# Kernel optimization log

Hardware: AMD Instinct MI355X
Metric: run time of the kernel (lower is better)

The kernel has to match this reference:

```python
import jax, jax.numpy as jnp
import numpy as np

N_NODES = 100000
N_EDGES = 600000
NODE_IN = 387
HID = 128
EDGE_DIM = 7


def _p(key, shape, scale=0.02):
    return jax.random.normal(key, shape, dtype=jnp.float32) * scale


def setup_inputs() -> dict:
    key = jax.random.key(0)
    ks = jax.random.split(key, 24)
    x = jax.random.normal(ks[0], (N_NODES, NODE_IN), dtype=jnp.float32)
    edge_index = jax.random.randint(ks[1], (2, N_EDGES), 0, N_NODES, dtype=jnp.int64)
    edge_attr = jax.random.normal(ks[2], (N_EDGES, EDGE_DIM), dtype=jnp.float32)
    return {
        "x": x,
        "edge_index": edge_index,
        "edge_attr": edge_attr,
        # conv1: edge lin (7 -> 387), mlp (387 -> 128 -> 128)
        "e1_w": _p(ks[3], (EDGE_DIM, NODE_IN)), "e1_b": jnp.zeros((NODE_IN,), jnp.float32),
        "m1_w1": _p(ks[4], (NODE_IN, HID)), "m1_b1": jnp.zeros((HID,), jnp.float32),
        "m1_w2": _p(ks[5], (HID, HID)), "m1_b2": jnp.zeros((HID,), jnp.float32),
        # conv2: edge lin (7 -> 128), mlp (128 -> 128 -> 128)
        "e2_w": _p(ks[6], (EDGE_DIM, HID)), "e2_b": jnp.zeros((HID,), jnp.float32),
        "m2_w1": _p(ks[7], (HID, HID)), "m2_b1": jnp.zeros((HID,), jnp.float32),
        "m2_w2": _p(ks[8], (HID, HID)), "m2_b2": jnp.zeros((HID,), jnp.float32),
        # edge_mlp: (2*128+7 -> 128 -> 2); dropout is identity at eval
        "em_w1": _p(ks[9], (2 * HID + EDGE_DIM, HID)), "em_b1": jnp.zeros((HID,), jnp.float32),
        "em_w2": _p(ks[10], (HID, 2)), "em_b2": jnp.zeros((2,), jnp.float32),
    }


def gine_conv(x, src, dst, edge_attr, ew, eb, w1, b1, w2, b2, eps=0.0):
    # message: relu(x_j + Lin(edge_attr)); aggregate sum at destination
    msg = jax.nn.relu(x[src] + edge_attr @ ew + eb)  # [E, D]
    aggr = jax.ops.segment_sum(msg, dst, num_segments=x.shape[0])  # [N, D]
    h = (1.0 + eps) * x + aggr
    return jax.nn.relu(h @ w1 + b1) @ w2 + b2


def reference(x, edge_index, edge_attr,
              e1_w, e1_b, m1_w1, m1_b1, m1_w2, m1_b2,
              e2_w, e2_b, m2_w1, m2_b1, m2_w2, m2_b2,
              em_w1, em_b1, em_w2, em_b2):
    src, dst = edge_index[0], edge_index[1]
    h = gine_conv(x, src, dst, edge_attr, e1_w, e1_b, m1_w1, m1_b1, m1_w2, m1_b2)
    h = jax.nn.relu(h)
    h = gine_conv(h, src, dst, edge_attr, e2_w, e2_b, m2_w1, m2_b1, m2_w2, m2_b2)
    h = jax.nn.relu(h)
    edge_input = jnp.concatenate([h[src], h[dst], edge_attr], axis=1)  # [E, 263]
    return jax.nn.relu(edge_input @ em_w1 + em_b1) @ em_w2 + em_b2  # [E, 2]
```

## Files before the change

kernel.cpp:

```cpp
#include <hip/hip_runtime.h>


using f32x4 = __attribute__((ext_vector_type(4))) float;
using s16x8 = __attribute__((ext_vector_type(8))) short;

#define N_NODES 100000
#define N_EDGES 600000
#define NODE_IN 387
#define KPAD    416
#define HID     128
#define NB_SCAN 391

__device__ __forceinline__ unsigned short f2bf(float f) {
    unsigned u = __float_as_uint(f);
    u += 0x7FFFu + ((u >> 16) & 1u);
    return (unsigned short)(u >> 16);
}
__device__ __forceinline__ float bf2f(short h) {
    return __uint_as_float(((unsigned)(unsigned short)h) << 16);
}

__global__ __launch_bounds__(256) void k_decode(const unsigned* __restrict__ w,
                                                int* __restrict__ s32,
                                                int* __restrict__ d32) {
    __shared__ unsigned long long bs[4];
    __shared__ int is64_s;
    const int t = threadIdx.x;
    unsigned any = 0;
    for (int i = 1 + 2 * t; i < 2048; i += 512) any |= w[i];
    unsigned long long b = __ballot(any != 0);
    if ((t & 63) == 0) bs[t >> 6] = b;
    __syncthreads();
    if (t == 0) is64_s = ((bs[0] | bs[1] | bs[2] | bs[3]) == 0ULL) ? 1 : 0;
    __syncthreads();
    const int is64 = is64_s;
    const int e = blockIdx.x * 256 + t;
    if (e < N_EDGES) {
        if (is64) {
            s32[e] = (int)w[2 * e];
            d32[e] = (int)w[2 * N_EDGES + 2 * e];
        } else {
            s32[e] = (int)w[e];
            d32[e] = (int)w[N_EDGES + e];
        }
    }
}

__global__ __launch_bounds__(256) void k_prep(const float* __restrict__ w1,
                                              const float* __restrict__ w2,
                                              const float* __restrict__ v1,
                                              const float* __restrict__ v2,
                                              const float* __restrict__ ew1,
                                              unsigned short* __restrict__ W1t,
                                              unsigned short* __restrict__ W2t,
                                              unsigned short* __restrict__ V1t,
                                              unsigned short* __restrict__ V2t,
                                              unsigned short* __restrict__ EW1t) {
    int i = blockIdx.x * 256 + threadIdx.x;
    if (i < 128 * KPAD) {
        int c = i / KPAD, k = i - c * KPAD;
        W1t[i] = (k < NODE_IN) ? f2bf(w1[k * HID + c]) : (unsigned short)0;
        return;
    }
    i -= 128 * KPAD;
    if (i < 16384) { int c = i >> 7, k = i & 127; W2t[i] = f2bf(w2[k * HID + c]); return; }
    i -= 16384;
    if (i < 16384) { int c = i >> 7, k = i & 127; V1t[i] = f2bf(v1[k * HID + c]); return; }
    i -= 16384;
    if (i < 16384) { int c = i >> 7, k = i & 127; V2t[i] = f2bf(v2[k * HID + c]); return; }
    i -= 16384;
    if (i < 32768) { int c = i >> 8, k = i & 255; EW1t[i] = f2bf(ew1[k * HID + c]); return; }
}

__global__ __launch_bounds__(256) void k_castx(const float* __restrict__ x,
                                               unsigned short* __restrict__ xbf) {
    const int g = blockIdx.x * 256 + threadIdx.x;
    if (g >= N_NODES * 52) return;
    const int row = g / 52, c0 = (g - row * 52) * 8;
    s16x8 v;
#pragma unroll
    for (int j = 0; j < 8; ++j) {
        const int c = c0 + j;
        v[j] = (c < NODE_IN) ? (short)f2bf(x[row * NODE_IN + c]) : (short)0;
    }
    *(s16x8*)&xbf[row * KPAD + c0] = v;
}

__global__ __launch_bounds__(256) void k_hist(const int* __restrict__ d32,
                                              int* __restrict__ cnt) {
    const int e = blockIdx.x * 256 + threadIdx.x;
    if (e < N_EDGES) atomicAdd(&cnt[d32[e]], 1);
}

__global__ __launch_bounds__(256) void k_scanA(const int* __restrict__ cnt,
                                               int* __restrict__ bsum) {
    __shared__ int wt[4];
    const int t = threadIdx.x;
    const int i = blockIdx.x * 256 + t;
    int v = (i < N_NODES) ? cnt[i] : 0;
#pragma unroll
    for (int off = 32; off; off >>= 1) v += __shfl_down(v, off);
    if ((t & 63) == 0) wt[t >> 6] = v;
    __syncthreads();
    if (t == 0) bsum[blockIdx.x] = wt[0] + wt[1] + wt[2] + wt[3];
}

__global__ __launch_bounds__(256) void k_scanC(int* __restrict__ cnt,
                                               const int* __restrict__ bsum) {
    __shared__ int wt[4];
    __shared__ int wt2[4];
    __shared__ int sh_bofs;
    const int t = threadIdx.x, b = blockIdx.x;
    int accp = 0;
    for (int i = t; i < NB_SCAN; i += 256) if (i < b) accp += bsum[i];
#pragma unroll
    for (int off = 32; off; off >>= 1) accp += __shfl_down(accp, off);
    if ((t & 63) == 0) wt[t >> 6] = accp;
    __syncthreads();
    if (t == 0) sh_bofs = wt[0] + wt[1] + wt[2] + wt[3];
    const int i = b * 256 + t;
    const int v = (i < N_NODES) ? cnt[i] : 0;
    int inc = v;
    const int lane = t & 63;
#pragma unroll
    for (int off = 1; off < 64; off <<= 1) {
        int u = __shfl_up(inc, off);
        if (lane >= off) inc += u;
    }
    if (lane == 63) wt2[t >> 6] = inc;
    __syncthreads();
    int wbase = 0;
    for (int wI = 0; wI < (t >> 6); ++wI) wbase += wt2[wI];
    if (i < N_NODES) cnt[i] = sh_bofs + wbase + inc - v;
}

__global__ __launch_bounds__(256) void k_scatter(const int* __restrict__ s32,
                                                 const int* __restrict__ d32,
                                                 const float* __restrict__ ea,
                                                 int* __restrict__ cur,
                                                 int* __restrict__ ss2,
                                                 int* __restrict__ ds2,
                                                 float* __restrict__ eas) {
    const int e = blockIdx.x * 256 + threadIdx.x;
    if (e < N_EDGES) {
        const int d = d32[e];
        const int pos = atomicAdd(&cur[d], 1);
        ss2[pos] = s32[e];
        ds2[pos] = d;
#pragma unroll
        for (int q = 0; q < 7; ++q) eas[pos * 8 + q] = ea[e * 7 + q];
        eas[pos * 8 + 7] = 0.f;
    }
}

#define STAGE_B(dst, srcbase, stride_) do {                                   \
    const int col_ = t >> 1, h_ = t & 1;                                      \
    *(s16x8*)&(dst)[col_ * 40 + h_ * 16] =                                    \
        *(const s16x8*)&(srcbase)[col_ * (stride_) + h_ * 16];                \
    *(s16x8*)&(dst)[col_ * 40 + h_ * 16 + 8] =                                \
        *(const s16x8*)&(srcbase)[col_ * (stride_) + h_ * 16 + 8];            \
} while (0)

__global__ __launch_bounds__(256) void k_edge1(const unsigned short* __restrict__ xbf,
                                               const int* __restrict__ ss2,
                                               const int* __restrict__ ds2,
                                               const float* __restrict__ eas,
                                               const float* __restrict__ e1w,
                                               const float* __restrict__ e1b,
                                               const unsigned short* __restrict__ W1t,
                                               float* __restrict__ yagg) {
    __shared__ __align__(16) char pool[31232];
    unsigned short* Asm = (unsigned short*)(pool);
    unsigned short* Bsm = (unsigned short*)(pool + 5120);
    float* e1w_s = (float*)(pool + 15360);
    float* e1b_s = (float*)(pool + 27008);
    float* ea_s  = (float*)(pool + 28672);
    int* ss_s    = (int*)(pool + 30720);
    int* dst_s   = (int*)(pool + 30976);
    float* Csm   = (float*)(pool);

    const int t = threadIdx.x;
    const int e0 = blockIdx.x * 64;

    if (t < 64) ss_s[t] = ss2[e0 + t];
    else if (t < 128) dst_s[t - 64] = ds2[e0 + (t - 64)];
    for (int i = t; i < 7 * KPAD; i += 256) {
        int q = i / KPAD, k = i - q * KPAD;
        e1w_s[i] = (k < NODE_IN) ? e1w[q * NODE_IN + k] : 0.f;
    }
    for (int i = t; i < KPAD; i += 256) e1b_s[i] = (i < NODE_IN) ? e1b[i] : 0.f;
    for (int i = t; i < 512; i += 256) ea_s[i] = eas[e0 * 8 + i];
    __syncthreads();

    const int lane = t & 63, wid = t >> 6;
    const int wr = wid >> 1, wc = wid & 1;
    const int r = t >> 2, kc = (t & 3) * 8;
    const int srow = ss_s[r];
    float eav[7];
#pragma unroll
    for (int q = 0; q < 7; ++q) eav[q] = ea_s[r * 8 + q];

    f32x4 acc[2][4];
    const f32x4 zero = {0.f, 0.f, 0.f, 0.f};
#pragma unroll
    for (int mi = 0; mi < 2; ++mi)
#pragma unroll
        for (int ni = 0; ni < 4; ++ni) acc[mi][ni] = zero;

    s16x8 xa_n = *(const s16x8*)&xbf[srow * KPAD + kc];
    for (int ks = 0; ks < 13; ++ks) {
        const s16x8 xa = xa_n;
        if (ks < 12) xa_n = *(const s16x8*)&xbf[srow * KPAD + (ks + 1) * 32 + kc];
        {
            const int kb = ks * 32 + kc;
            s16x8 v;
#pragma unroll
            for (int j = 0; j < 8; ++j) {
                const int k = kb + j;
                float le = e1b_s[k];
#pragma unroll
                for (int q = 0; q < 7; ++q) le = fmaf(eav[q], e1w_s[q * KPAD + k], le);
                v[j] = (short)f2bf(fmaxf(bf2f(xa[j]) + le, 0.f));
            }
            *(s16x8*)&Asm[r * 40 + kc] = v;
        }
        STAGE_B(Bsm, &W1t[ks * 32], KPAD);
        __syncthreads();
        const int koff = (lane >> 4) * 8;
        const int rA = lane & 15;
        s16x8 a0 = *(const s16x8*)&Asm[(wr * 32 + rA) * 40 + koff];
        s16x8 a1 = *(const s16x8*)&Asm[(wr * 32 + 16 + rA) * 40 + koff];
#pragma unroll
        for (int ni = 0; ni < 4; ++ni) {
            s16x8 b = *(const s16x8*)&Bsm[(wc * 64 + ni * 16 + rA) * 40 + koff];
            acc[0][ni] = __builtin_amdgcn_mfma_f32_16x16x32_bf16(a0, b, acc[0][ni], 0, 0, 0);
            acc[1][ni] = __builtin_amdgcn_mfma_f32_16x16x32_bf16(a1, b, acc[1][ni], 0, 0, 0);
        }
        __syncthreads();
    }
    const int g = lane >> 4;
    const int cb = wc * 64 + (lane & 15);
#pragma unroll
    for (int p = 0; p < 2; ++p) {
        if (wr == p) {
#pragma unroll
            for (int mi = 0; mi < 2; ++mi)
#pragma unroll
                for (int reg = 0; reg < 4; ++reg) {
                    const int row = mi * 16 + g * 4 + reg;
#pragma unroll
                    for (int ni = 0; ni < 4; ++ni)
                        Csm[row * 129 + cb + ni * 16] = acc[mi][ni][reg];
                }
        }
        __syncthreads();
        if (t < 128) {
            const int base = p * 32;
            float s = 0.f;
            int prev = dst_s[base];
            for (int rr = 0; rr < 32; ++rr) {
                const int d = dst_s[base + rr];
                const float v = Csm[rr * 129 + t];
                if (d != prev) { atomicAdd(&yagg[prev * HID + t], s); s = 0.f; prev = d; }
                s += v;
            }
            atomicAdd(&yagg[prev * HID + t], s);
        }
        __syncthreads();
    }
}

__global__ __launch_bounds__(256) void k_node1(const unsigned short* __restrict__ xbf,
                                               const float* __restrict__ yagg,
                                               const unsigned short* __restrict__ W1t,
                                               const unsigned short* __restrict__ W2t,
                                               const float* __restrict__ b1,
                                               const float* __restrict__ b2,
                                               unsigned short* __restrict__ r1b) {
    __shared__ __align__(16) unsigned short Asm[64 * 40];
    __shared__ __align__(16) unsigned short Bsm[128 * 40];
    __shared__ __align__(16) unsigned short Hsm[64 * 136];
    const int t = threadIdx.x;
    const int i0 = blockIdx.x * 64;
    const int lane = t & 63, wid = t >> 6, wr = wid >> 1, wc = wid & 1;
    const int r = t >> 2, kc = (t & 3) * 8;
    const int rg = i0 + r;
    const bool rvalid = rg < N_NODES;

    f32x4 acc[2][4];
    const f32x4 zero = {0.f, 0.f, 0.f, 0.f};
#pragma unroll
    for (int mi = 0; mi < 2; ++mi)
#pragma unroll
        for (int ni = 0; ni < 4; ++ni) acc[mi][ni] = zero;

    for (int ks = 0; ks < 13; ++ks) {
        {
            s16x8 v;
            if (rvalid) v = *(const s16x8*)&xbf[rg * KPAD + ks * 32 + kc];
            else {
#pragma unroll
                for (int j = 0; j < 8; ++j) v[j] = 0;
            }
            *(s16x8*)&Asm[r * 40 + kc] = v;
        }
        STAGE_B(Bsm, &W1t[ks * 32], KPAD);
        __syncthreads();
        const int koff = (lane >> 4) * 8;
        const int rA = lane & 15;
        s16x8 a0 = *(const s16x8*)&Asm[(wr * 32 + rA) * 40 + koff];
        s16x8 a1 = *(const s16x8*)&Asm[(wr * 32 + 16 + rA) * 40 + koff];
#pragma unroll
        for (int ni = 0; ni < 4; ++ni) {
            s16x8 b = *(const s16x8*)&Bsm[(wc * 64 + ni * 16 + rA) * 40 + koff];
            acc[0][ni] = __builtin_amdgcn_mfma_f32_16x16x32_bf16(a0, b, acc[0][ni], 0, 0, 0);
            acc[1][ni] = __builtin_amdgcn_mfma_f32_16x16x32_bf16(a1, b, acc[1][ni], 0, 0, 0);
        }
        __syncthreads();
    }
    const int jb = wc * 64 + (lane & 15);
#pragma unroll
    for (int mi = 0; mi < 2; ++mi) {
#pragma unroll
        for (int reg = 0; reg < 4; ++reg) {
            const int rloc = wr * 32 + mi * 16 + (lane >> 4) * 4 + reg;
            const int rowg = i0 + rloc;
#pragma unroll
            for (int ni = 0; ni < 4; ++ni) {
                const int j = jb + ni * 16;
                float v = acc[mi][ni][reg];
                if (rowg < N_NODES) {
                    v += yagg[rowg * HID + j] + b1[j];
                    v = fmaxf(v, 0.f);
                } else v = 0.f;
                Hsm[rloc * 136 + j] = f2bf(v);
            }
        }
    }
    __syncthreads();
    f32x4 acc2[2][4];
#pragma unroll
    for (int mi = 0; mi < 2; ++mi)
#pragma unroll
        for (int ni = 0; ni < 4; ++ni) acc2[mi][ni] = zero;

    for (int ks = 0; ks < 4; ++ks) {
        STAGE_B(Bsm, &W2t[ks * 32], HID);
        __syncthreads();
        const int koff = (lane >> 4) * 8;
        const int rA = lane & 15;
        s16x8 a0 = *(const s16x8*)&Hsm[(wr * 32 + rA) * 136 + ks * 32 + koff];
        s16x8 a1 = *(const s16x8*)&Hsm[(wr * 32 + 16 + rA) * 136 + ks * 32 + koff];
#pragma unroll
        for (int ni = 0; ni < 4; ++ni) {
            s16x8 b = *(const s16x8*)&Bsm[(wc * 64 + ni * 16 + rA) * 40 + koff];
            acc2[0][ni] = __builtin_amdgcn_mfma_f32_16x16x32_bf16(a0, b, acc2[0][ni], 0, 0, 0);
            acc2[1][ni] = __builtin_amdgcn_mfma_f32_16x16x32_bf16(a1, b, acc2[1][ni], 0, 0, 0);
        }
        __syncthreads();
    }
#pragma unroll
    for (int mi = 0; mi < 2; ++mi) {
#pragma unroll
        for (int reg = 0; reg < 4; ++reg) {
            const int rloc = wr * 32 + mi * 16 + (lane >> 4) * 4 + reg;
            const int rowg = i0 + rloc;
            if (rowg < N_NODES) {
#pragma unroll
                for (int ni = 0; ni < 4; ++ni) {
                    const int j = jb + ni * 16;
                    float v = acc2[mi][ni][reg] + b2[j];
                    r1b[rowg * HID + j] = f2bf(fmaxf(v, 0.f));
                }
            }
        }
    }
}

__global__ __launch_bounds__(256) void k_edge2(const unsigned short* __restrict__ r1b,
                                               const int* __restrict__ ss2,
                                               const int* __restrict__ ds2,
                                               const float* __restrict__ eas,
                                               const float* __restrict__ e2w,
                                               const float* __restrict__ e2b,
                                               float* __restrict__ agg2) {
    __shared__ float w_s[7 * HID];
    __shared__ float b_s[HID];
    __shared__ float Csm[64 * 129];
    __shared__ float ea_s[64 * 8];
    __shared__ int ss_s[64];
    __shared__ int ds_s[64];
    const int t = threadIdx.x;
    const int e0 = blockIdx.x * 64;
    for (int i = t; i < 7 * HID; i += 256) w_s[i] = e2w[i];
    if (t < HID) b_s[t] = e2b[t];
    if (t < 64) ss_s[t] = ss2[e0 + t];
    else if (t < 128) ds_s[t - 64] = ds2[e0 + (t - 64)];
    for (int i = t; i < 512; i += 256) ea_s[i] = eas[e0 * 8 + i];
    __syncthreads();

    const int r = t >> 2, c0 = (t & 3) * 32;
    const int s = ss_s[r];
    float eav[7];
#pragma unroll
    for (int q = 0; q < 7; ++q) eav[q] = ea_s[r * 8 + q];
    const s16x8* rp = (const s16x8*)&r1b[s * HID + c0];
#pragma unroll
    for (int u = 0; u < 4; ++u) {
        s16x8 hv = rp[u];
#pragma unroll
        for (int j = 0; j < 8; ++j) {
            const int c = c0 + u * 8 + j;
            float v = bf2f(hv[j]) + b_s[c];
#pragma unroll
            for (int q = 0; q < 7; ++q) v = fmaf(eav[q], w_s[q * HID + c], v);
            Csm[r * 129 + c] = fmaxf(v, 0.f);
        }
    }
    __syncthreads();
    if (t < 128) {
        float ssum = 0.f;
        int prev = ds_s[0];
        for (int rr = 0; rr < 64; ++rr) {
            const int d = ds_s[rr];
            const float v = Csm[rr * 129 + t];
            if (d != prev) { atomicAdd(&agg2[prev * HID + t], ssum); ssum = 0.f; prev = d; }
            ssum += v;
        }
        atomicAdd(&agg2[prev * HID + t], ssum);
    }
}

__global__ __launch_bounds__(256) void k_node2(const unsigned short* __restrict__ r1b,
                                               const float* __restrict__ agg2,
                                               const unsigned short* __restrict__ V1t,
                                               const unsigned short* __restrict__ V2t,
                                               const float* __restrict__ b1,
                                               const float* __restrict__ b2,
                                               unsigned short* __restrict__ r2) {
    __shared__ __align__(16) unsigned short Asm[64 * 40];
    __shared__ __align__(16) unsigned short Bsm[128 * 40];
    __shared__ __align__(16) unsigned short Hsm[64 * 136];
    const int t = threadIdx.x;
    const int i0 = blockIdx.x * 64;
    const int lane = t & 63, wid = t >> 6, wr = wid >> 1, wc = wid & 1;
    const int r = t >> 2, kc = (t & 3) * 8;
    const int rg = i0 + r;
    const bool rvalid = rg < N_NODES;

    f32x4 acc[2][4];
    const f32x4 zero = {0.f, 0.f, 0.f, 0.f};
#pragma unroll
    for (int mi = 0; mi < 2; ++mi)
#pragma unroll
        for (int ni = 0; ni < 4; ++ni) acc[mi][ni] = zero;

    for (int ks = 0; ks < 4; ++ks) {
        {
            const int kb = ks * 32 + kc;
            s16x8 v;
            if (rvalid) {
                const s16x8 ra = *(const s16x8*)&r1b[rg * HID + kb];
                const f32x4* pb = (const f32x4*)&agg2[rg * HID + kb];
                f32x4 w0 = pb[0], w1 = pb[1];
#pragma unroll
                for (int j = 0; j < 4; ++j) v[j] = (short)f2bf(bf2f(ra[j]) + w0[j]);
#pragma unroll
                for (int j = 0; j < 4; ++j) v[4 + j] = (short)f2bf(bf2f(ra[4 + j]) + w1[j]);
            } else {
#pragma unroll
                for (int j = 0; j < 8; ++j) v[j] = 0;
            }
            *(s16x8*)&Asm[r * 40 + kc] = v;
        }
        STAGE_B(Bsm, &V1t[ks * 32], HID);
        __syncthreads();
        const int koff = (lane >> 4) * 8;
        const int rA = lane & 15;
        s16x8 a0 = *(const s16x8*)&Asm[(wr * 32 + rA) * 40 + koff];
        s16x8 a1 = *(const s16x8*)&Asm[(wr * 32 + 16 + rA) * 40 + koff];
#pragma unroll
        for (int ni = 0; ni < 4; ++ni) {
            s16x8 b = *(const s16x8*)&Bsm[(wc * 64 + ni * 16 + rA) * 40 + koff];
            acc[0][ni] = __builtin_amdgcn_mfma_f32_16x16x32_bf16(a0, b, acc[0][ni], 0, 0, 0);
            acc[1][ni] = __builtin_amdgcn_mfma_f32_16x16x32_bf16(a1, b, acc[1][ni], 0, 0, 0);
        }
        __syncthreads();
    }
    const int jb = wc * 64 + (lane & 15);
#pragma unroll
    for (int mi = 0; mi < 2; ++mi) {
#pragma unroll
        for (int reg = 0; reg < 4; ++reg) {
            const int rloc = wr * 32 + mi * 16 + (lane >> 4) * 4 + reg;
            const int rowg = i0 + rloc;
#pragma unroll
            for (int ni = 0; ni < 4; ++ni) {
                const int j = jb + ni * 16;
                float v = acc[mi][ni][reg];
                if (rowg < N_NODES) {
                    v += b1[j];
                    v = fmaxf(v, 0.f);
                } else v = 0.f;
                Hsm[rloc * 136 + j] = f2bf(v);
            }
        }
    }
    __syncthreads();
    f32x4 acc2[2][4];
#pragma unroll
    for (int mi = 0; mi < 2; ++mi)
#pragma unroll
        for (int ni = 0; ni < 4; ++ni) acc2[mi][ni] = zero;

    for (int ks = 0; ks < 4; ++ks) {
        STAGE_B(Bsm, &V2t[ks * 32], HID);
        __syncthreads();
        const int koff = (lane >> 4) * 8;
        const int rA = lane & 15;
        s16x8 a0 = *(const s16x8*)&Hsm[(wr * 32 + rA) * 136 + ks * 32 + koff];
        s16x8 a1 = *(const s16x8*)&Hsm[(wr * 32 + 16 + rA) * 136 + ks * 32 + koff];
#pragma unroll
        for (int ni = 0; ni < 4; ++ni) {
            s16x8 b = *(const s16x8*)&Bsm[(wc * 64 + ni * 16 + rA) * 40 + koff];
            acc2[0][ni] = __builtin_amdgcn_mfma_f32_16x16x32_bf16(a0, b, acc2[0][ni], 0, 0, 0);
            acc2[1][ni] = __builtin_amdgcn_mfma_f32_16x16x32_bf16(a1, b, acc2[1][ni], 0, 0, 0);
        }
        __syncthreads();
    }
#pragma unroll
    for (int mi = 0; mi < 2; ++mi) {
#pragma unroll
        for (int reg = 0; reg < 4; ++reg) {
            const int rloc = wr * 32 + mi * 16 + (lane >> 4) * 4 + reg;
            const int rowg = i0 + rloc;
            if (rowg < N_NODES) {
#pragma unroll
                for (int ni = 0; ni < 4; ++ni) {
                    const int j = jb + ni * 16;
                    float v = acc2[mi][ni][reg] + b2[j];
                    r2[rowg * HID + j] = f2bf(fmaxf(v, 0.f));
                }
            }
        }
    }
}

__global__ __launch_bounds__(256) void k_head(const unsigned short* __restrict__ r2,
                                              const int* __restrict__ srcp,
                                              const int* __restrict__ dstp,
                                              const float* __restrict__ ea,
                                              const unsigned short* __restrict__ EW1t,
                                              const float* __restrict__ emw1,
                                              const float* __restrict__ emb1,
                                              const float* __restrict__ emw2,
                                              const float* __restrict__ emb2,
                                              float* __restrict__ out) {
    __shared__ __align__(16) unsigned short Asm[64 * 40];
    __shared__ __align__(16) unsigned short Bsm[128 * 40];
    __shared__ float Hsm[64 * 129];
    __shared__ float ew_ea[7 * HID];
    __shared__ float eb1_s[HID];
    __shared__ float w2_s[256];
    __shared__ float b2_s[2];
    __shared__ float ea_s[64 * 8];
    __shared__ int src_s[64];
    __shared__ int dst_s[64];
    __shared__ float red[512];
    const int t = threadIdx.x;
    const int e0 = blockIdx.x * 64;

    for (int i = t; i < 7 * HID; i += 256) ew_ea[i] = emw1[256 * HID + i];
    if (t < HID) eb1_s[t] = emb1[t];
    if (t < 256) w2_s[t] = emw2[t];
    if (t < 2) b2_s[t] = emb2[t];
    for (int i = t; i < 64 * 7; i += 256) {
        int r = i / 7, q = i - r * 7;
        ea_s[r * 8 + q] = ea[(e0 + r) * 7 + q];
    }
    if (t < 64) src_s[t] = srcp[e0 + t];
    else if (t < 128) dst_s[t - 64] = dstp[e0 + (t - 64)];
    __syncthreads();

    const int lane = t & 63, wid = t >> 6, wr = wid >> 1, wc = wid & 1;
    const int r = t >> 2, kc = (t & 3) * 8;

    f32x4 acc[2][4];
    const f32x4 zero = {0.f, 0.f, 0.f, 0.f};
#pragma unroll
    for (int mi = 0; mi < 2; ++mi)
#pragma unroll
        for (int ni = 0; ni < 4; ++ni) acc[mi][ni] = zero;

    for (int ks = 0; ks < 8; ++ks) {
        {
            const int k = ks * 32 + kc;
            const unsigned short* p = (k < HID) ? &r2[src_s[r] * HID + k]
                                                : &r2[dst_s[r] * HID + (k - HID)];
            *(s16x8*)&Asm[r * 40 + kc] = *(const s16x8*)p;
        }
        STAGE_B(Bsm, &EW1t[ks * 32], 256);
        __syncthreads();
        const int koff = (lane >> 4) * 8;
        const int rA = lane & 15;
        s16x8 a0 = *(const s16x8*)&Asm[(wr * 32 + rA) * 40 + koff];
        s16x8 a1 = *(const s16x8*)&Asm[(wr * 32 + 16 + rA) * 40 + koff];
#pragma unroll
        for (int ni = 0; ni < 4; ++ni) {
            s16x8 b = *(const s16x8*)&Bsm[(wc * 64 + ni * 16 + rA) * 40 + koff];
            acc[0][ni] = __builtin_amdgcn_mfma_f32_16x16x32_bf16(a0, b, acc[0][ni], 0, 0, 0);
            acc[1][ni] = __builtin_amdgcn_mfma_f32_16x16x32_bf16(a1, b, acc[1][ni], 0, 0, 0);
        }
        __syncthreads();
    }
    const int jb = wc * 64 + (lane & 15);
#pragma unroll
    for (int mi = 0; mi < 2; ++mi) {
#pragma unroll
        for (int reg = 0; reg < 4; ++reg) {
            const int rloc = wr * 32 + mi * 16 + (lane >> 4) * 4 + reg;
#pragma unroll
            for (int ni = 0; ni < 4; ++ni) {
                const int j = jb + ni * 16;
                float v = acc[mi][ni][reg] + eb1_s[j];
#pragma unroll
                for (int q = 0; q < 7; ++q)
                    v = fmaf(ea_s[rloc * 8 + q], ew_ea[q * HID + j], v);
                Hsm[rloc * 129 + j] = fmaxf(v, 0.f);
            }
        }
    }
    __syncthreads();
    {
        const int e = t & 63, p = t >> 6;
        const float* hb = &Hsm[e * 129 + p * 32];
        float s0 = 0.f, s1 = 0.f;
#pragma unroll
        for (int j = 0; j < 32; ++j) {
            const float h = hb[j];
            s0 = fmaf(h, w2_s[(p * 32 + j) * 2], s0);
            s1 = fmaf(h, w2_s[(p * 32 + j) * 2 + 1], s1);
        }
        red[(e * 4 + p) * 2] = s0;
        red[(e * 4 + p) * 2 + 1] = s1;
    }
    __syncthreads();
    if (t < 64) {
        float o0 = b2_s[0], o1 = b2_s[1];
#pragma unroll
        for (int p = 0; p < 4; ++p) {
            o0 += red[(t * 4 + p) * 2];
            o1 += red[(t * 4 + p) * 2 + 1];
        }
        out[(e0 + t) * 2] = o0;
        out[(e0 + t) * 2 + 1] = o1;
    }
}

extern "C" void kernel_launch(void* const* d_in, const int* in_sizes, int n_in,
                              void* d_out, int out_size, void* d_ws, size_t ws_size,
                              hipStream_t stream) {
    (void)in_sizes; (void)n_in; (void)out_size; (void)ws_size;
    const float* x    = (const float*)d_in[0];
    const unsigned* eidx = (const unsigned*)d_in[1];
    const float* ea   = (const float*)d_in[2];
    const float* e1w  = (const float*)d_in[3];
    const float* e1b  = (const float*)d_in[4];
    const float* m1w1 = (const float*)d_in[5];
    const float* m1b1 = (const float*)d_in[6];
    const float* m1w2 = (const float*)d_in[7];
    const float* m1b2 = (const float*)d_in[8];
    const float* e2w  = (const float*)d_in[9];
    const float* e2b  = (const float*)d_in[10];
    const float* m2w1 = (const float*)d_in[11];
    const float* m2b1 = (const float*)d_in[12];
    const float* m2w2 = (const float*)d_in[13];
    const float* m2b2 = (const float*)d_in[14];
    const float* emw1 = (const float*)d_in[15];
    const float* emb1 = (const float*)d_in[16];
    const float* emw2 = (const float*)d_in[17];
    const float* emb2 = (const float*)d_in[18];
    float* out = (float*)d_out;

    char* ws = (char*)d_ws;
    float* yagg = (float*)(ws + 0);
    unsigned short* r1b = (unsigned short*)(ws + 51200000);
    unsigned short* r2  = (unsigned short*)(ws + 76800000);
    float* eas          = (float*)(ws + 76800000);
    unsigned short* xbf = (unsigned short*)(ws + 102400000);
    unsigned short* W1t  = (unsigned short*)(ws + 185600000);
    unsigned short* W2t  = (unsigned short*)(ws + 185706496);
    unsigned short* V1t  = (unsigned short*)(ws + 185739264);
    unsigned short* V2t  = (unsigned short*)(ws + 185772032);
    unsigned short* EW1t = (unsigned short*)(ws + 185804800);
    int* s32  = (int*)(ws + 185870336);
    int* d32  = (int*)(ws + 188270336);
    int* ss2  = (int*)(ws + 190670336);
    int* ds2  = (int*)(ws + 193070336);
    int* cnt  = (int*)(ws + 195470336);
    int* bsum = (int*)(ws + 195870336);

    hipMemsetAsync(yagg, 0, (size_t)N_NODES * HID * 4, stream);
    hipMemsetAsync(cnt, 0, (size_t)N_NODES * 4, stream);
    k_decode<<<2344, 256, 0, stream>>>(eidx, s32, d32);
    k_prep<<<528, 256, 0, stream>>>(m1w1, m1w2, m2w1, m2w2, emw1, W1t, W2t, V1t, V2t, EW1t);
    k_castx<<<(N_NODES * 52 + 255) / 256, 256, 0, stream>>>(x, xbf);
    k_hist<<<2344, 256, 0, stream>>>(d32, cnt);
    k_scanA<<<NB_SCAN, 256, 0, stream>>>(cnt, bsum);
    k_scanC<<<NB_SCAN, 256, 0, stream>>>(cnt, bsum);
    k_scatter<<<2344, 256, 0, stream>>>(s32, d32, ea, cnt, ss2, ds2, eas);
    k_edge1<<<N_EDGES / 64, 256, 0, stream>>>(xbf, ss2, ds2, eas, e1w, e1b, W1t, yagg);
    k_node1<<<(N_NODES + 63) / 64, 256, 0, stream>>>(xbf, yagg, W1t, W2t, m1b1, m1b2, r1b);
    hipMemsetAsync(yagg, 0, (size_t)N_NODES * HID * 4, stream);
    k_edge2<<<N_EDGES / 64, 256, 0, stream>>>(r1b, ss2, ds2, eas, e2w, e2b, yagg);
    k_node2<<<(N_NODES + 63) / 64, 256, 0, stream>>>(r1b, yagg, V1t, V2t, m2b1, m2b2, r2);
    k_head<<<N_EDGES / 64, 256, 0, stream>>>(r2, s32, d32, ea, EW1t, emw1, emb1, emw2, emb2, out);
}
```

Measured before the change: 1.076 ms.

## Compute edge-attr linear terms with MFMA instead of scalar FMA loops

Packs the 7-wide edge-attribute weights plus bias into padded bf16 matrices in the prep kernel. In k_edge1 and k_head, the per-element scalar FMA loops over edge attributes are replaced with small MFMA products, using an augmented [ea, 1] row so the bias is folded in. This removes the per-block staging of fp32 edge weights and a lot of VALU work. It also splits the segmented atomic reduction in k_edge1 across all 256 threads instead of 128. The cost is extra syncs per k-step and bf16 rounding of the edge-attr weights and bias, which were fp32 before.

Result: faster. 924.6 us (-14.1%).

```diff
diff --git a/kernel.cpp b/kernel.cpp
--- a/kernel.cpp
+++ b/kernel.cpp
@@ -51,11 +51,16 @@
                                               const float* __restrict__ v1,
                                               const float* __restrict__ v2,
                                               const float* __restrict__ ew1,
+                                              const float* __restrict__ e1w,
+                                              const float* __restrict__ e1b,
+                                              const float* __restrict__ emb1,
                                               unsigned short* __restrict__ W1t,
                                               unsigned short* __restrict__ W2t,
                                               unsigned short* __restrict__ V1t,
                                               unsigned short* __restrict__ V2t,
-                                              unsigned short* __restrict__ EW1t) {
+                                              unsigned short* __restrict__ EW1t,
+                                              unsigned short* __restrict__ E1T,
+                                              unsigned short* __restrict__ EWeaT) {
     int i = blockIdx.x * 256 + threadIdx.x;
     if (i < 128 * KPAD) {
         int c = i / KPAD, k = i - c * KPAD;
@@ -70,6 +75,26 @@
     if (i < 16384) { int c = i >> 7, k = i & 127; V2t[i] = f2bf(v2[k * HID + c]); return; }
     i -= 16384;
     if (i < 32768) { int c = i >> 8, k = i & 255; EW1t[i] = f2bf(ew1[k * HID + c]); return; }
+    i -= 32768;
+    if (i < 416 * 32) {
+        int f = i >> 5, q = i & 31;
+        unsigned short v = 0;
+        if (f < NODE_IN) {
+            if (q < 7) v = f2bf(e1w[q * NODE_IN + f]);
+            else if (q == 7) v = f2bf(e1b[f]);
+        }
+        E1T[i] = v;
+        return;
+    }
+    i -= 416 * 32;
+    if (i < 128 * 32) {
+        int c = i >> 5, q = i & 31;
+        unsigned short v = 0;
+        if (q < 7) v = f2bf(ew1[(256 + q) * HID + c]);
+        else if (q == 7) v = f2bf(emb1[c]);
+        EWeaT[i] = v;
+        return;
+    }
 }
 
 __global__ __launch_bounds__(256) void k_castx(const float* __restrict__ x,
@@ -165,41 +190,47 @@
                                                const int* __restrict__ ss2,
                                                const int* __restrict__ ds2,
                                                const float* __restrict__ eas,
-                                               const float* __restrict__ e1w,
-                                               const float* __restrict__ e1b,
+                                               const unsigned short* __restrict__ E1T,
                                                const unsigned short* __restrict__ W1t,
                                                float* __restrict__ yagg) {
-    __shared__ __align__(16) char pool[31232];
-    unsigned short* Asm = (unsigned short*)(pool);
-    unsigned short* Bsm = (unsigned short*)(pool + 5120);
-    float* e1w_s = (float*)(pool + 15360);
-    float* e1b_s = (float*)(pool + 27008);
-    float* ea_s  = (float*)(pool + 28672);
-    int* ss_s    = (int*)(pool + 30720);
-    int* dst_s   = (int*)(pool + 30976);
-    float* Csm   = (float*)(pool);
+    __shared__ __align__(16) char pool[26880];
+    unsigned short* Asm  = (unsigned short*)(pool);
+    unsigned short* Bsm  = (unsigned short*)(pool + 5120);
+    unsigned short* Bsm2 = (unsigned short*)(pool + 15360);
+    float* le_lds = (float*)(pool + 17920);
+    int* ss_s     = (int*)(pool + 26368);
+    int* dst_s    = (int*)(pool + 26624);
+    float* Csm    = (float*)(pool);
 
     const int t = threadIdx.x;
     const int e0 = blockIdx.x * 64;
 
     if (t < 64) ss_s[t] = ss2[e0 + t];
     else if (t < 128) dst_s[t - 64] = ds2[e0 + (t - 64)];
-    for (int i = t; i < 7 * KPAD; i += 256) {
-        int q = i / KPAD, k = i - q * KPAD;
-        e1w_s[i] = (k < NODE_IN) ? e1w[q * NODE_IN + k] : 0.f;
-    }
-    for (int i = t; i < KPAD; i += 256) e1b_s[i] = (i < NODE_IN) ? e1b[i] : 0.f;
-    for (int i = t; i < 512; i += 256) ea_s[i] = eas[e0 * 8 + i];
-    __syncthreads();
 
     const int lane = t & 63, wid = t >> 6;
     const int wr = wid >> 1, wc = wid & 1;
     const int r = t >> 2, kc = (t & 3) * 8;
+    const int rA = lane & 15;
+    const int koff = (lane >> 4) * 8;
+
+    {
+        s16x8 v;
+#pragma unroll
+        for (int j = 0; j < 8; ++j) v[j] = 0;
+        if (kc == 0) {
+#pragma unroll
+            for (int q = 0; q < 7; ++q) v[q] = (short)f2bf(eas[(e0 + r) * 8 + q]);
+            v[7] = (short)0x3F80;
+        }
+        *(s16x8*)&Asm[r * 40 + kc] = v;
+    }
+    __syncthreads();
+    const s16x8 eap0 = *(const s16x8*)&Asm[(wr * 32 + rA) * 40 + koff];
+    const s16x8 eap1 = *(const s16x8*)&Asm[(wr * 32 + 16 + rA) * 40 + koff];
+    __syncthreads();
+
     const int srow = ss_s[r];
-    float eav[7];
-#pragma unroll
-    for (int q = 0; q < 7; ++q) eav[q] = ea_s[r * 8 + q];
-
     f32x4 acc[2][4];
     const f32x4 zero = {0.f, 0.f, 0.f, 0.f};
 #pragma unroll
@@ -211,23 +242,34 @@
     for (int ks = 0; ks < 13; ++ks) {
         const s16x8 xa = xa_n;
         if (ks < 12) xa_n = *(const s16x8*)&xbf[srow * KPAD + (ks + 1) * 32 + kc];
+        STAGE_B(Bsm, &W1t[ks * 32], KPAD);
+        if (t < 128) {
+            const int n = t >> 2, qg = (t & 3) * 8;
+            *(s16x8*)&Bsm2[n * 40 + qg] = *(const s16x8*)&E1T[(ks * 32 + n) * 32 + qg];
+        }
+        __syncthreads();
         {
-            const int kb = ks * 32 + kc;
+            s16x8 b2 = *(const s16x8*)&Bsm2[(wc * 16 + rA) * 40 + koff];
+            f32x4 le0 = __builtin_amdgcn_mfma_f32_16x16x32_bf16(eap0, b2, zero, 0, 0, 0);
+            f32x4 le1 = __builtin_amdgcn_mfma_f32_16x16x32_bf16(eap1, b2, zero, 0, 0, 0);
+            const int cw = wc * 16 + rA;
+#pragma unroll
+            for (int reg = 0; reg < 4; ++reg) {
+                const int row = wr * 32 + (lane >> 4) * 4 + reg;
+                le_lds[row * 33 + cw] = le0[reg];
+                le_lds[(row + 16) * 33 + cw] = le1[reg];
+            }
+        }
+        __syncthreads();
+        {
+            const float* lep = &le_lds[r * 33 + kc];
             s16x8 v;
 #pragma unroll
-            for (int j = 0; j < 8; ++j) {
-                const int k = kb + j;
-                float le = e1b_s[k];
-#pragma unroll
-                for (int q = 0; q < 7; ++q) le = fmaf(eav[q], e1w_s[q * KPAD + k], le);
-                v[j] = (short)f2bf(fmaxf(bf2f(xa[j]) + le, 0.f));
-            }
+            for (int j = 0; j < 8; ++j)
+                v[j] = (short)f2bf(fmaxf(bf2f(xa[j]) + lep[j], 0.f));
             *(s16x8*)&Asm[r * 40 + kc] = v;
         }
-        STAGE_B(Bsm, &W1t[ks * 32], KPAD);
-        __syncthreads();
-        const int koff = (lane >> 4) * 8;
-        const int rA = lane & 15;
+        __syncthreads();
         s16x8 a0 = *(const s16x8*)&Asm[(wr * 32 + rA) * 40 + koff];
         s16x8 a1 = *(const s16x8*)&Asm[(wr * 32 + 16 + rA) * 40 + koff];
 #pragma unroll
@@ -238,8 +280,8 @@
         }
         __syncthreads();
     }
-    const int g = lane >> 4;
-    const int cb = wc * 64 + (lane & 15);
+    const int gq = lane >> 4;
+    const int cb = wc * 64 + rA;
 #pragma unroll
     for (int p = 0; p < 2; ++p) {
         if (wr == p) {
@@ -247,24 +289,25 @@
             for (int mi = 0; mi < 2; ++mi)
 #pragma unroll
                 for (int reg = 0; reg < 4; ++reg) {
-                    const int row = mi * 16 + g * 4 + reg;
+                    const int row = mi * 16 + gq * 4 + reg;
 #pragma unroll
                     for (int ni = 0; ni < 4; ++ni)
                         Csm[row * 129 + cb + ni * 16] = acc[mi][ni][reg];
                 }
         }
         __syncthreads();
-        if (t < 128) {
-            const int base = p * 32;
+        {
+            const int col = t & 127, half = t >> 7;
+            const int b0 = p * 32 + half * 16;
             float s = 0.f;
-            int prev = dst_s[base];
-            for (int rr = 0; rr < 32; ++rr) {
-                const int d = dst_s[base + rr];
-                const float v = Csm[rr * 129 + t];
-                if (d != prev) { atomicAdd(&yagg[prev * HID + t], s); s = 0.f; prev = d; }
+            int prev = dst_s[b0];
+            for (int rr = 0; rr < 16; ++rr) {
+                const int d = dst_s[b0 + rr];
+                const float v = Csm[(half * 16 + rr) * 129 + col];
+                if (d != prev) { atomicAdd(&yagg[prev * HID + col], s); s = 0.f; prev = d; }
                 s += v;
             }
-            atomicAdd(&yagg[prev * HID + t], s);
+            atomicAdd(&yagg[prev * HID + col], s);
         }
         __syncthreads();
     }
@@ -551,46 +594,58 @@
                                               const int* __restrict__ dstp,
                                               const float* __restrict__ ea,
                                               const unsigned short* __restrict__ EW1t,
-                                              const float* __restrict__ emw1,
-                                              const float* __restrict__ emb1,
+                                              const unsigned short* __restrict__ EWeaT,
                                               const float* __restrict__ emw2,
                                               const float* __restrict__ emb2,
                                               float* __restrict__ out) {
     __shared__ __align__(16) unsigned short Asm[64 * 40];
     __shared__ __align__(16) unsigned short Bsm[128 * 40];
     __shared__ float Hsm[64 * 129];
-    __shared__ float ew_ea[7 * HID];
-    __shared__ float eb1_s[HID];
     __shared__ float w2_s[256];
     __shared__ float b2_s[2];
-    __shared__ float ea_s[64 * 8];
     __shared__ int src_s[64];
     __shared__ int dst_s[64];
     __shared__ float red[512];
     const int t = threadIdx.x;
     const int e0 = blockIdx.x * 64;
 
-    for (int i = t; i < 7 * HID; i += 256) ew_ea[i] = emw1[256 * HID + i];
-    if (t < HID) eb1_s[t] = emb1[t];
     if (t < 256) w2_s[t] = emw2[t];
     if (t < 2) b2_s[t] = emb2[t];
-    for (int i = t; i < 64 * 7; i += 256) {
-        int r = i / 7, q = i - r * 7;
-        ea_s[r * 8 + q] = ea[(e0 + r) * 7 + q];
-    }
     if (t < 64) src_s[t] = srcp[e0 + t];
     else if (t < 128) dst_s[t - 64] = dstp[e0 + (t - 64)];
-    __syncthreads();
 
     const int lane = t & 63, wid = t >> 6, wr = wid >> 1, wc = wid & 1;
     const int r = t >> 2, kc = (t & 3) * 8;
+    const int rA = lane & 15;
+    const int koff = (lane >> 4) * 8;
+
+    {
+        s16x8 v;
+#pragma unroll
+        for (int j = 0; j < 8; ++j) v[j] = 0;
+        if (kc == 0) {
+#pragma unroll
+            for (int q = 0; q < 7; ++q) v[q] = (short)f2bf(ea[(e0 + r) * 7 + q]);
+            v[7] = (short)0x3F80;
+        }
+        *(s16x8*)&Asm[r * 40 + kc] = v;
+    }
+    STAGE_B(Bsm, EWeaT, 32);
+    __syncthreads();
 
     f32x4 acc[2][4];
     const f32x4 zero = {0.f, 0.f, 0.f, 0.f};
-#pragma unroll
-    for (int mi = 0; mi < 2; ++mi)
-#pragma unroll
-        for (int ni = 0; ni < 4; ++ni) acc[mi][ni] = zero;
+    {
+        const s16x8 eap0 = *(const s16x8*)&Asm[(wr * 32 + rA) * 40 + koff];
+        const s16x8 eap1 = *(const s16x8*)&Asm[(wr * 32 + 16 + rA) * 40 + koff];
+#pragma unroll
+        for (int ni = 0; ni < 4; ++ni) {
+            s16x8 b = *(const s16x8*)&Bsm[(wc * 64 + ni * 16 + rA) * 40 + koff];
+            acc[0][ni] = __builtin_amdgcn_mfma_f32_16x16x32_bf16(eap0, b, zero, 0, 0, 0);
+            acc[1][ni] = __builtin_amdgcn_mfma_f32_16x16x32_bf16(eap1, b, zero, 0, 0, 0);
+        }
+    }
+    __syncthreads();
 
     for (int ks = 0; ks < 8; ++ks) {
         {
@@ -601,8 +656,6 @@
         }
         STAGE_B(Bsm, &EW1t[ks * 32], 256);
         __syncthreads();
-        const int koff = (lane >> 4) * 8;
-        const int rA = lane & 15;
         s16x8 a0 = *(const s16x8*)&Asm[(wr * 32 + rA) * 40 + koff];
         s16x8 a1 = *(const s16x8*)&Asm[(wr * 32 + 16 + rA) * 40 + koff];
 #pragma unroll
@@ -613,21 +666,15 @@
         }
         __syncthreads();
     }
-    const int jb = wc * 64 + (lane & 15);
+    const int jb = wc * 64 + rA;
 #pragma unroll
     for (int mi = 0; mi < 2; ++mi) {
 #pragma unroll
         for (int reg = 0; reg < 4; ++reg) {
             const int rloc = wr * 32 + mi * 16 + (lane >> 4) * 4 + reg;
 #pragma unroll
-            for (int ni = 0; ni < 4; ++ni) {
-                const int j = jb + ni * 16;
-                float v = acc[mi][ni][reg] + eb1_s[j];
-#pragma unroll
-                for (int q = 0; q < 7; ++q)
-                    v = fmaf(ea_s[rloc * 8 + q], ew_ea[q * HID + j], v);
-                Hsm[rloc * 129 + j] = fmaxf(v, 0.f);
-            }
+            for (int ni = 0; ni < 4; ++ni)
+                Hsm[rloc * 129 + jb + ni * 16] = fmaxf(acc[mi][ni][reg], 0.f);
         }
     }
     __syncthreads();
@@ -688,31 +735,35 @@
     unsigned short* r2  = (unsigned short*)(ws + 76800000);
     float* eas          = (float*)(ws + 76800000);
     unsigned short* xbf = (unsigned short*)(ws + 102400000);
-    unsigned short* W1t  = (unsigned short*)(ws + 185600000);
-    unsigned short* W2t  = (unsigned short*)(ws + 185706496);
-    unsigned short* V1t  = (unsigned short*)(ws + 185739264);
-    unsigned short* V2t  = (unsigned short*)(ws + 185772032);
-    unsigned short* EW1t = (unsigned short*)(ws + 185804800);
-    int* s32  = (int*)(ws + 185870336);
-    int* d32  = (int*)(ws + 188270336);
-    int* ss2  = (int*)(ws + 190670336);
-    int* ds2  = (int*)(ws + 193070336);
-    int* cnt  = (int*)(ws + 195470336);
-    int* bsum = (int*)(ws + 195870336);
+    unsigned short* W1t   = (unsigned short*)(ws + 185600000);
+    unsigned short* W2t   = (unsigned short*)(ws + 185706496);
+    unsigned short* V1t   = (unsigned short*)(ws + 185739264);
+    unsigned short* V2t   = (unsigned short*)(ws + 185772032);
+    unsigned short* EW1t  = (unsigned short*)(ws + 185804800);
+    unsigned short* E1T   = (unsigned short*)(ws + 185870336);
+    unsigned short* EWeaT = (unsigned short*)(ws + 185896960);
+    int* s32  = (int*)(ws + 185905152);
+    int* d32  = (int*)(ws + 188305152);
+    int* ss2  = (int*)(ws + 190705152);
+    int* ds2  = (int*)(ws + 193105152);
+    int* cnt  = (int*)(ws + 195505152);
+    int* bsum = (int*)(ws + 195905152);
 
     hipMemsetAsync(yagg, 0, (size_t)N_NODES * HID * 4, stream);
     hipMemsetAsync(cnt, 0, (size_t)N_NODES * 4, stream);
     k_decode<<<2344, 256, 0, stream>>>(eidx, s32, d32);
-    k_prep<<<528, 256, 0, stream>>>(m1w1, m1w2, m2w1, m2w2, emw1, W1t, W2t, V1t, V2t, EW1t);
+    k_prep<<<596, 256, 0, stream>>>(m1w1, m1w2, m2w1, m2w2, emw1, e1w, e1b, emb1,
+                                    W1t, W2t, V1t, V2t, EW1t, E1T, EWeaT);
     k_castx<<<(N_NODES * 52 + 255) / 256, 256, 0, stream>>>(x, xbf);
     k_hist<<<2344, 256, 0, stream>>>(d32, cnt);
     k_scanA<<<NB_SCAN, 256, 0, stream>>>(cnt, bsum);
     k_scanC<<<NB_SCAN, 256, 0, stream>>>(cnt, bsum);
     k_scatter<<<2344, 256, 0, stream>>>(s32, d32, ea, cnt, ss2, ds2, eas);
-    k_edge1<<<N_EDGES / 64, 256, 0, stream>>>(xbf, ss2, ds2, eas, e1w, e1b, W1t, yagg);
+    k_edge1<<<N_EDGES / 64, 256, 0, stream>>>(xbf, ss2, ds2, eas, E1T, W1t, yagg);
     k_node1<<<(N_NODES + 63) / 64, 256, 0, stream>>>(xbf, yagg, W1t, W2t, m1b1, m1b2, r1b);
     hipMemsetAsync(yagg, 0, (size_t)N_NODES * HID * 4, stream);
     k_edge2<<<N_EDGES / 64, 256, 0, stream>>>(r1b, ss2, ds2, eas, e2w, e2b, yagg);
     k_node2<<<(N_NODES + 63) / 64, 256, 0, stream>>>(r1b, yagg, V1t, V2t, m2b1, m2b2, r2);
-    k_head<<<N_EDGES / 64, 256, 0, stream>>>(r2, s32, d32, ea, EW1t, emw1, emb1, emw2, emb2, out);
-}
+    k_head<<<N_EDGES / 64, 256, 0, stream>>>(r2, s32, d32, ea, EW1t, EWeaT,
+                                             emw2, emb2, out);
+}
```
